# Optimization experiments

Measured on AMD Instinct MI355X. Metric: run time of the kernel, lower is better.

The kernel has to match this reference:

```python
import jax, jax.numpy as jnp
import numpy as np

E = 16      # num_experts
K = 4       # num_experts_per_tok
H = 2048    # hidden_size
I = 1408    # moe_intermediate_size
SI = 5632   # shared expert intermediate size
CAP = 1024
NORM_TOPK = False


def setup_inputs() -> dict:
    key = jax.random.key(0)
    ks = jax.random.split(key, 9)
    def w(k, shape, fan_in):
        return jax.random.normal(k, shape, jnp.float32) * (fan_in ** -0.5)
    return {
        "hidden_states": jax.random.normal(ks[0], (1, 2048, H), jnp.float32),
        "gate_w":  w(ks[1], (E, H), H),        # router: Linear(H -> E), no bias
        "we_gate": w(ks[2], (E, I, H), H),     # per-expert gate_proj weights
        "we_up":   w(ks[3], (E, I, H), H),     # per-expert up_proj weights
        "we_down": w(ks[4], (E, H, I), I),     # per-expert down_proj weights
        "ws_gate": w(ks[5], (SI, H), H),       # shared expert gate_proj
        "ws_up":   w(ks[6], (SI, H), H),       # shared expert up_proj
        "ws_down": w(ks[7], (H, SI), SI),      # shared expert down_proj
        "sg_w":    w(ks[8], (1, H), H),        # shared_expert_gate: Linear(H -> 1)
    }


def reference(hidden_states, gate_w, we_gate, we_up, we_down,
              ws_gate, ws_up, ws_down, sg_w):
    B, S, Hd = hidden_states.shape
    x = hidden_states.reshape(-1, Hd)                      # [T, H]
    T = x.shape[0]

    # --- router ---
    router_logits = x @ gate_w.T                           # [T, E]
    probs = jax.nn.softmax(router_logits.astype(jnp.float32), axis=-1)
    topw, topi = jax.lax.top_k(probs, K)                   # [T, K]
    if NORM_TOPK:
        topw = topw / topw.sum(axis=-1, keepdims=True)

    # --- dispatch: flatten (token, slot) assignments ---
    A = T * K
    fe = topi.reshape(A)                                   # expert id per assignment
    fw = topw.reshape(A)                                   # routing weight per assignment
    ft = jnp.repeat(jnp.arange(T), K)                      # token id per assignment
    # position of each assignment within its expert (rank in arrival order)
    oh = jax.nn.one_hot(fe, E, dtype=jnp.int32)            # [A, E]
    pos = jnp.take_along_axis(jnp.cumsum(oh, axis=0) - 1, fe[:, None], axis=1)[:, 0]
    valid = pos < CAP
    # scatter tokens into per-expert buffers; overflow goes to dummy row CAP
    buf = jnp.zeros((E, CAP + 1, Hd), x.dtype)
    buf = buf.at[fe, jnp.where(valid, pos, CAP)].set(x[ft])[:, :CAP]  # [E, C, H]

    # --- per-expert SiLU-gated MLP (batched grouped GEMMs) ---
    g = jnp.einsum('ech,eih->eci', buf, we_gate)
    u = jnp.einsum('ech,eih->eci', buf, we_up)
    eo = jnp.einsum('eci,ehi->ech', jax.nn.silu(g) * u, we_down)      # [E, C, H]

    # --- combine: weighted scatter-add back to tokens ---
    ga = eo[fe, jnp.minimum(pos, CAP - 1)]                 # [A, H]
    wcomb = (fw * valid.astype(fw.dtype)).astype(x.dtype)
    y = jnp.zeros((T, Hd), x.dtype).at[ft].add(ga * wcomb[:, None])

    # --- shared expert with sigmoid gate ---
    sh = (jax.nn.silu(x @ ws_gate.T) * (x @ ws_up.T)) @ ws_down.T
    sh = jax.nn.sigmoid(x @ sg_w.T) * sh

    out = (y + sh).reshape(B, S, Hd)
    return out, router_logits
```

## Files before the change

kernel.cpp:

```cpp
#include <hip/hip_runtime.h>

#define T_TOK 2048
#define NE 16
#define KTOP 4
#define HD 2048
#define ID 1408
#define SID 5632
#define CAPACITY 1024

typedef __attribute__((ext_vector_type(8))) short short8;
typedef __attribute__((ext_vector_type(4))) float floatx4;

__device__ __forceinline__ short f2b(float f){
  union { float f; unsigned u; } v; v.f = f;
  unsigned r = v.u + 0x7fffu + ((v.u >> 16) & 1u);
  return (short)(r >> 16);
}
__device__ __forceinline__ float b2f(short s){
  union { float f; unsigned u; } v; v.u = ((unsigned)(unsigned short)s) << 16;
  return v.f;
}
__device__ __forceinline__ unsigned cvt_pk(float a, float b){
  unsigned r;
  asm("v_cvt_pk_bf16_f32 %0, %1, %2" : "=v"(r) : "v"(a), "v"(b));
  return r;
}
__device__ __forceinline__ short8 cvt8(float4 a, float4 b){
  union { unsigned d[4]; short8 s; } u;
  u.d[0] = cvt_pk(a.x, a.y); u.d[1] = cvt_pk(a.z, a.w);
  u.d[2] = cvt_pk(b.x, b.y); u.d[3] = cvt_pk(b.z, b.w);
  return u.s;
}
__device__ __forceinline__ void gl16(const void* g, void* l){
  __builtin_amdgcn_global_load_lds(
      (const __attribute__((address_space(1))) void*)g,
      (__attribute__((address_space(3))) void*)l, 16, 0, 0);
}

__device__ __forceinline__ void conv_range(
    int cb, int ncb,
    const float* __restrict__ s1, short* __restrict__ d1, long long n1,
    const float* __restrict__ s2, short* __restrict__ d2, long long n2)
{
  const long long tot = n1 + n2;
  const long long stride = (long long)ncb * 256;
  #pragma unroll 2
  for (long long i = (long long)cb * 256 + threadIdx.x; i < tot; i += stride){
    const float* s; short8* d; long long j;
    if (i < n1){ s = s1; d = (short8*)d1; j = i; }
    else       { s = s2; d = (short8*)d2; j = i - n1; }
    float4 f0 = ((const float4*)s)[j * 2];
    float4 f1 = ((const float4*)s)[j * 2 + 1];
    d[j] = cvt8(f0, f1);
  }
}

__global__ void moe_zero(int* __restrict__ counts){
  if (threadIdx.x < NE) counts[threadIdx.x] = 0;
}

__global__ void moe_router(const float* __restrict__ x,
                           const float* __restrict__ gate_w,
                           const float* __restrict__ sg_w,
                           float* __restrict__ logits_out,
                           short* __restrict__ xb,
                           int* __restrict__ counts,
                           int* __restrict__ slot_token,
                           int* __restrict__ tslot,
                           float* __restrict__ tw,
                           float* __restrict__ sg,
                           const float* cs1, short* cd1, long long cn1,
                           const float* cs2, short* cd2, long long cn2)
{
  if (blockIdx.x >= 512){
    conv_range(blockIdx.x - 512, gridDim.x - 512, cs1, cd1, cn1, cs2, cd2, cn2);
    return;
  }
  int wave = threadIdx.x >> 6, lane = threadIdx.x & 63;
  int t = (blockIdx.x << 2) + wave;
  const float4* xr = (const float4*)(x + (size_t)t * HD);
  short8* xbw = (short8*)(xb + (size_t)t * HD);
  float acc[17];
  #pragma unroll
  for (int e = 0; e < 17; ++e) acc[e] = 0.f;
  #pragma unroll
  for (int j = 0; j < 4; ++j){
    int i4 = (j * 64 + lane) * 2;
    float4 x0 = xr[i4], x1 = xr[i4 + 1];
    xbw[j * 64 + lane] = cvt8(x0, x1);
    #pragma unroll
    for (int e = 0; e < 16; ++e){
      const float4* gr = (const float4*)(gate_w + e * HD);
      float4 g0 = gr[i4], g1 = gr[i4 + 1];
      acc[e] += x0.x*g0.x + x0.y*g0.y + x0.z*g0.z + x0.w*g0.w
              + x1.x*g1.x + x1.y*g1.y + x1.z*g1.z + x1.w*g1.w;
    }
    const float4* sr = (const float4*)sg_w;
    float4 s0 = sr[i4], s1 = sr[i4 + 1];
    acc[16] += x0.x*s0.x + x0.y*s0.y + x0.z*s0.z + x0.w*s0.w
             + x1.x*s1.x + x1.y*s1.y + x1.z*s1.z + x1.w*s1.w;
  }
  #pragma unroll
  for (int e = 0; e < 17; ++e){
    float v = acc[e];
    #pragma unroll
    for (int off = 32; off > 0; off >>= 1) v += __shfl_xor(v, off, 64);
    acc[e] = v;
  }
  if (lane == 0){
    float m = acc[0];
    #pragma unroll
    for (int e = 1; e < 16; ++e) m = fmaxf(m, acc[e]);
    float p[16]; float s = 0.f;
    #pragma unroll
    for (int e = 0; e < 16; ++e){ p[e] = expf(acc[e] - m); s += p[e]; }
    float inv = 1.f / s;
    #pragma unroll
    for (int e = 0; e < 16; ++e) logits_out[t * 16 + e] = acc[e];
    unsigned used = 0;
    for (int k = 0; k < KTOP; ++k){
      float best = -1.f; int bi = 0;
      #pragma unroll
      for (int e = 0; e < 16; ++e){
        float pe = ((used >> e) & 1u) ? -1.f : p[e];
        if (pe > best){ best = pe; bi = e; }
      }
      used |= (1u << bi);
      int pos = atomicAdd(&counts[bi], 1);
      int enc = -1;
      if (pos < CAPACITY){
        slot_token[bi * CAPACITY + pos] = t;
        enc = bi * CAPACITY + pos;
      }
      tslot[t * KTOP + k] = enc;
      tw[t * KTOP + k] = best * inv;
    }
    sg[t] = 1.f / (1.f + expf(-acc[16]));
  }
}


#define GEMM_PREAMBLE \
  const int tid = threadIdx.x; \
  const int lane = tid & 63, wave = tid >> 6; \
  const int wr = wave >> 1, wc = wave & 1; \
  const int lrow = lane & 15, lk = lane >> 4; \
  const int s_th = (tid & 7) ^ ((tid >> 3) & 7); \
  const int koff = (s_th & 3) << 3; \
  const int rloc = ((tid >> 3) << 1) + (s_th >> 2); \
  const int lb = lrow >> 1; \
  const int soff = (((((lrow & 1) << 2) | lk) ^ (lb & 7)) << 4); \
  const int abase = (wr * 32 + lb) * 128 + soff;

#define WAIT8  asm volatile("s_waitcnt vmcnt(8)" ::: "memory");
#define WAIT6  asm volatile("s_waitcnt vmcnt(6)" ::: "memory");
#define WAIT4  asm volatile("s_waitcnt vmcnt(4)" ::: "memory");
#define WAIT3  asm volatile("s_waitcnt vmcnt(3)" ::: "memory");
#define WAIT0  asm volatile("s_waitcnt vmcnt(0)" ::: "memory");
#define SBAR   asm volatile("s_barrier" ::: "memory");

__global__ __launch_bounds__(256) void moe_gateup(
    const short* __restrict__ Asrc,
    const short* __restrict__ Wg, const short* __restrict__ Wu,
    short* __restrict__ Out,
    const int* __restrict__ counts, const int* __restrict__ slot_token,
    int Ndim, int Kdim, int expert_mode, int mtiles, int ntiles,
    const float* cs1, short* cd1, long long cn1,
    const float* cs2, short* cd2, long long cn2, int conv_nwg)
{
  if ((int)blockIdx.x < conv_nwg){
    conv_range(blockIdx.x, conv_nwg, cs1, cd1, cn1, cs2, cd2, cn2);
    return;
  }
  int nwg = gridDim.x - conv_nwg;
  int bid = blockIdx.x - conv_nwg;
  int wg = ((bid & 7) * (nwg >> 3)) + (bid >> 3);
  int m_t = wg % mtiles; wg /= mtiles;
  int n_t = wg % ntiles; int e = wg / ntiles;

  int cnt = T_TOK; size_t woff = 0; short* out = Out;
  if (expert_mode){
    cnt = counts[e]; if (cnt > CAPACITY) cnt = CAPACITY;
    if (m_t * 128 >= cnt) return;
    woff = (size_t)e * Ndim * Kdim;
    out = Out + (size_t)e * CAPACITY * Ndim;
  }
  const int m0 = m_t * 128, n0 = n_t * 64;

  __shared__ __align__(16) char smem[3][16384];

  GEMM_PREAMBLE
  const int gbase = 8192 + (wc * 16 + lb) * 128 + soff;

  const short* aP0;
  const short* aP1;
  {
    int p0 = m0 + rloc, p1 = m0 + 64 + rloc;
    if (expert_mode){
      int q0 = (p0 < cnt) ? p0 : 0, q1 = (p1 < cnt) ? p1 : 0;
      aP0 = Asrc + (size_t)slot_token[e * CAPACITY + q0] * Kdim + koff;
      aP1 = Asrc + (size_t)slot_token[e * CAPACITY + q1] * Kdim + koff;
    } else {
      aP0 = Asrc + (size_t)p0 * Kdim + koff;
      aP1 = Asrc + (size_t)p1 * Kdim + koff;
    }
  }
  const short* bgP = Wg + woff + (size_t)(n0 + rloc) * Kdim + koff;
  const short* buP = Wu + woff + (size_t)(n0 + rloc) * Kdim + koff;

  const floatx4 vzero = {0.f, 0.f, 0.f, 0.f};
  floatx4 accg[4][2], accu[4][2];
  #pragma unroll
  for (int i = 0; i < 4; ++i)
    #pragma unroll
    for (int j = 0; j < 2; ++j){ accg[i][j] = vzero; accu[i][j] = vzero; }

#define GU_ISSUE(B, T) { char* _b = (B); const int _k = (T) << 5; \
    gl16(aP0 + _k, _b + tid * 16); \
    gl16(aP1 + _k, _b + 4096 + tid * 16); \
    gl16(bgP + _k, _b + 8192 + tid * 16); \
    gl16(buP + _k, _b + 12288 + tid * 16); }

#define GU_COMPUTE(B) { const char* bb = (B); \
    short8 a[4], bg[2], bu[2]; \
    _Pragma("unroll") \
    for (int mf = 0; mf < 4; ++mf) a[mf] = *(const short8*)(bb + abase + mf * 1024); \
    _Pragma("unroll") \
    for (int nf = 0; nf < 2; ++nf){ \
      bg[nf] = *(const short8*)(bb + gbase + nf * 1024); \
      bu[nf] = *(const short8*)(bb + gbase + 4096 + nf * 1024); } \
    __builtin_amdgcn_s_setprio(1); \
    _Pragma("unroll") \
    for (int mf = 0; mf < 4; ++mf) \
      _Pragma("unroll") \
      for (int nf = 0; nf < 2; ++nf){ \
        accg[mf][nf] = __builtin_amdgcn_mfma_f32_16x16x32_bf16(a[mf], bg[nf], accg[mf][nf], 0, 0, 0); \
        accu[mf][nf] = __builtin_amdgcn_mfma_f32_16x16x32_bf16(a[mf], bu[nf], accu[mf][nf], 0, 0, 0); } \
    __builtin_amdgcn_s_setprio(0); }

  const int NSTEP = Kdim >> 5;
  char* b0 = smem[0];
  char* b1 = smem[1];
  char* b2 = smem[2];
  GU_ISSUE(b0, 0)
  GU_ISSUE(b1, 1)
  for (int s = 0; s < NSTEP; ++s){
    if (s + 2 < NSTEP){ GU_ISSUE(b2, s + 2) WAIT8 }
    else if (s + 2 == NSTEP){ WAIT4 }
    else { WAIT0 }
    SBAR
    GU_COMPUTE(b0)
    SBAR
    char* t = b0; b0 = b1; b1 = b2; b2 = t;
  }

  const int colbase = n0 + wc * 32 + lrow;
  #pragma unroll
  for (int mf = 0; mf < 4; ++mf){
    int pr = m0 + wr * 64 + mf * 16 + lk * 4;
    #pragma unroll
    for (int nf = 0; nf < 2; ++nf){
      floatx4 g4 = accg[mf][nf], u4 = accu[mf][nf];
      int col = colbase + nf * 16;
      #pragma unroll
      for (int r = 0; r < 4; ++r){
        float gv = g4[r], uv = u4[r];
        float a = (gv / (1.f + __expf(-gv))) * uv;
        out[(size_t)(pr + r) * Ndim + col] = f2b(a);
      }
    }
  }
}

template<int NF>
__global__ __launch_bounds__(256) void moe_down(
    const short* __restrict__ Asrc, const short* __restrict__ Wd,
    float* __restrict__ y, short* __restrict__ eo,
    const int* __restrict__ counts, const int* __restrict__ slot_token,
    const float* __restrict__ sgate,
    int Kdim, int expert_mode, int mtiles, int ntiles)
{
  int nwg = gridDim.x;
  int wg = ((blockIdx.x & 7) * (nwg >> 3)) + (blockIdx.x >> 3);
  int m_t = wg % mtiles; wg /= mtiles;
  int n_t = wg % ntiles; int e = wg / ntiles;

  int cnt = T_TOK; const short* ab = Asrc; size_t woff = 0;
  if (expert_mode){
    cnt = counts[e]; if (cnt > CAPACITY) cnt = CAPACITY;
    if (m_t * 128 >= cnt) return;
    ab = Asrc + (size_t)e * CAPACITY * Kdim;
    woff = (size_t)e * HD * Kdim;
  }
  const int m0 = m_t * 128, n0 = n_t * (NF * 32);

  __shared__ __align__(16) char smem[3][8192 + NF * 2048];

  GEMM_PREAMBLE
  const int bbase = 8192 + (wc * (NF * 8) + lb) * 128 + soff;

  const short* aP0 = ab + (size_t)(m0 + rloc) * Kdim + koff;
  const short* aP1 = ab + (size_t)(m0 + 64 + rloc) * Kdim + koff;
  const short* bP0 = Wd + woff + (size_t)(n0 + rloc) * Kdim + koff;
  const short* bP1 = (NF == 4) ? (Wd + woff + (size_t)(n0 + 64 + rloc) * Kdim + koff) : bP0;

  const floatx4 vzero = {0.f, 0.f, 0.f, 0.f};
  floatx4 acc[4][NF];
  #pragma unroll
  for (int i = 0; i < 4; ++i)
    #pragma unroll
    for (int j = 0; j < NF; ++j) acc[i][j] = vzero;

#define DN_ISSUE(B, T) { char* _b = (B); const int _k = (T) << 5; \
    gl16(aP0 + _k, _b + tid * 16); \
    gl16(aP1 + _k, _b + 4096 + tid * 16); \
    gl16(bP0 + _k, _b + 8192 + tid * 16); \
    if (NF == 4) gl16(bP1 + _k, _b + 12288 + tid * 16); }

#define DN_COMPUTE(B) { const char* bb = (B); \
    short8 a[4], b[NF]; \
    _Pragma("unroll") \
    for (int mf = 0; mf < 4; ++mf) a[mf] = *(const short8*)(bb + abase + mf * 1024); \
    _Pragma("unroll") \
    for (int nf = 0; nf < NF; ++nf) b[nf] = *(const short8*)(bb + bbase + nf * 1024); \
    __builtin_amdgcn_s_setprio(1); \
    _Pragma("unroll") \
    for (int mf = 0; mf < 4; ++mf) \
      _Pragma("unroll") \
      for (int nf = 0; nf < NF; ++nf) \
        acc[mf][nf] = __builtin_amdgcn_mfma_f32_16x16x32_bf16(a[mf], b[nf], acc[mf][nf], 0, 0, 0); \
    __builtin_amdgcn_s_setprio(0); }

  const int NSTEP = Kdim >> 5;
  char* b0 = smem[0];
  char* b1 = smem[1];
  char* b2 = smem[2];
  DN_ISSUE(b0, 0)
  DN_ISSUE(b1, 1)
  for (int s = 0; s < NSTEP; ++s){
    if (s + 2 < NSTEP){
      DN_ISSUE(b2, s + 2)
      if (NF == 4){ WAIT8 } else { WAIT6 }
    } else if (s + 2 == NSTEP){
      if (NF == 4){ WAIT4 } else { WAIT3 }
    } else { WAIT0 }
    SBAR
    DN_COMPUTE(b0)
    SBAR
    char* t = b0; b0 = b1; b1 = b2; b2 = t;
  }

  const int colb = n0 + wc * (NF * 16) + lrow;
  if (expert_mode){
    #pragma unroll
    for (int mf = 0; mf < 4; ++mf){
      int pr = m0 + wr * 64 + mf * 16 + lk * 4;
      #pragma unroll
      for (int r = 0; r < 4; ++r){
        int p = pr + r;
        #pragma unroll
        for (int nf = 0; nf < NF; ++nf)
          eo[(size_t)(e * CAPACITY + p) * HD + colb + nf * 16] = f2b(acc[mf][nf][r]);
      }
    }
  } else {
    #pragma unroll
    for (int mf = 0; mf < 4; ++mf){
      int pr = m0 + wr * 64 + mf * 16 + lk * 4;
      #pragma unroll
      for (int r = 0; r < 4; ++r){
        int t = pr + r;
        float sv = sgate[t];
        #pragma unroll
        for (int nf = 0; nf < NF; ++nf)
          y[(size_t)t * HD + colb + nf * 16] = sv * acc[mf][nf][r];
      }
    }
  }
}

__global__ void moe_combine(const short* __restrict__ eo,
                            const int* __restrict__ tslot,
                            const float* __restrict__ tw,
                            float* __restrict__ y)
{
  int t = blockIdx.x;
  int o = threadIdx.x << 3;
  float* yp = y + (size_t)t * HD + o;
  float4 a0 = *(const float4*)yp, a1 = *(const float4*)(yp + 4);
  float acc[8] = {a0.x, a0.y, a0.z, a0.w, a1.x, a1.y, a1.z, a1.w};
  #pragma unroll
  for (int k = 0; k < KTOP; ++k){
    int s = tslot[t * KTOP + k];
    if (s >= 0){
      float w = tw[t * KTOP + k];
      short8 v = *(const short8*)(eo + (size_t)s * HD + o);
      #pragma unroll
      for (int j = 0; j < 8; ++j) acc[j] += w * b2f(v[j]);
    }
  }
  float4 r0 = {acc[0], acc[1], acc[2], acc[3]};
  float4 r1 = {acc[4], acc[5], acc[6], acc[7]};
  *(float4*)yp = r0; *(float4*)(yp + 4) = r1;
}

extern "C" void kernel_launch(void* const* d_in, const int* in_sizes, int n_in,
                              void* d_out, int out_size, void* d_ws, size_t ws_size,
                              hipStream_t stream)
{
  (void)in_sizes; (void)n_in; (void)out_size; (void)ws_size;
  const float* x       = (const float*)d_in[0];
  const float* gate_w  = (const float*)d_in[1];
  const float* we_gate = (const float*)d_in[2];
  const float* we_up   = (const float*)d_in[3];
  const float* we_down = (const float*)d_in[4];
  const float* wsg     = (const float*)d_in[5];
  const float* wsu     = (const float*)d_in[6];
  const float* wsd     = (const float*)d_in[7];
  const float* sg_w    = (const float*)d_in[8];

  float* y      = (float*)d_out;
  float* logits = y + (size_t)T_TOK * HD;

  const size_t N_EW = (size_t)NE * ID * HD;
  const size_t N_SW = (size_t)SID * HD;
  const long long G_EW = (long long)(N_EW / 8);
  const long long G_SW = (long long)(N_SW / 8);

  char* ws = (char*)d_ws;
  size_t off = 0;
  short* xb   = (short*)(ws + off); off += (size_t)T_TOK * HD * 2;
  short* wb   = (short*)(ws + off); off += (3 * N_EW + 3 * N_SW) * 2;
  short* act  = (short*)(ws + off); off += (size_t)NE * CAPACITY * ID * 2;
  short* acts = (short*)(ws + off); off += (size_t)T_TOK * SID * 2;
  int*   slot_token = (int*)  (ws + off); off += 65536;
  int*   tslot      = (int*)  (ws + off); off += 32768;
  float* tw         = (float*)(ws + off); off += 32768;
  int*   counts     = (int*)  (ws + off); off += 256;
  float* sg         = (float*)(ws + off);

  short* wbeg = wb;
  short* wbeu = wb + N_EW;
  short* wbed = wb + 2 * N_EW;
  short* wbsg = wb + 3 * N_EW;
  short* wbsu = wb + 3 * N_EW + N_SW;
  short* wbsd = wb + 3 * N_EW + 2 * N_SW;
  short* eo = wbeg;

  moe_zero<<<1, 64, 0, stream>>>(counts);
  moe_router<<<512 + 512, 256, 0, stream>>>(x, gate_w, sg_w, logits, xb,
                                            counts, slot_token, tslot, tw, sg,
                                            wsg, wbsg, G_SW, wsu, wbsu, G_SW);
  moe_gateup<<<512 + 16 * 88, 256, 0, stream>>>(xb, wbsg, wbsu, acts,
                                                nullptr, nullptr, SID, HD, 0, 16, 88,
                                                we_gate, wbeg, G_EW, we_up, wbeu, G_EW, 512);
  moe_gateup<<<512 + 8 * 22 * NE, 256, 0, stream>>>(xb, wbeg, wbeu, act,
                                                    counts, slot_token, ID, HD, 1, 8, 22,
                                                    we_down, wbed, G_EW, wsd, wbsd, G_SW, 512);
  moe_down<2><<<16 * 32, 256, 0, stream>>>(acts, wbsd, y, nullptr, nullptr, nullptr,
                                           sg, SID, 0, 16, 32);
  moe_down<4><<<8 * 16 * NE, 256, 0, stream>>>(act, wbed, y, eo, counts, slot_token,
                                               nullptr, ID, 1, 8, 16);
  moe_combine<<<T_TOK, 256, 0, stream>>>(eo, tslot, tw, y);
}
```

Baseline: 760.5 us.

## Merge shared down-projection with expert gate/up into one launch, rebalance conversions

Reorganises the launch schedule. The shared-expert down-projection now runs in the same launch as the routed-expert gate/up GEMM and the expert down-weight conversion, and the shared down-weight fp32-to-bf16 conversion moves into the router launch. The down kernel is specialised to a 128-wide N tile, the count-zeroing kernel becomes a memset, and the number of launches drops. The aim is to cut launch gaps and tail underutilisation by overlapping independent work, at the cost of a mixed-workload grid whose block ordering determines load balance.

```diff
diff --git a/kernel.cpp b/kernel.cpp
--- a/kernel.cpp
+++ b/kernel.cpp
@@ -54,9 +54,24 @@
     d[j] = cvt8(f0, f1);
   }
 }
-
-__global__ void moe_zero(int* __restrict__ counts){
-  if (threadIdx.x < NE) counts[threadIdx.x] = 0;
+__device__ __forceinline__ void conv3(
+    int cb, int ncb,
+    const float* __restrict__ s1, short* __restrict__ d1, long long n1,
+    const float* __restrict__ s2, short* __restrict__ d2, long long n2,
+    const float* __restrict__ s3, short* __restrict__ d3, long long n3)
+{
+  const long long tot = n1 + n2 + n3;
+  const long long stride = (long long)ncb * 256;
+  #pragma unroll 2
+  for (long long i = (long long)cb * 256 + threadIdx.x; i < tot; i += stride){
+    const float* s; short8* d; long long j;
+    if (i < n1){ s = s1; d = (short8*)d1; j = i; }
+    else if (i < n1 + n2){ s = s2; d = (short8*)d2; j = i - n1; }
+    else { s = s3; d = (short8*)d3; j = i - n1 - n2; }
+    float4 f0 = ((const float4*)s)[j * 2];
+    float4 f1 = ((const float4*)s)[j * 2 + 1];
+    d[j] = cvt8(f0, f1);
+  }
 }
 
 __global__ void moe_router(const float* __restrict__ x,
@@ -70,10 +85,11 @@
                            float* __restrict__ tw,
                            float* __restrict__ sg,
                            const float* cs1, short* cd1, long long cn1,
-                           const float* cs2, short* cd2, long long cn2)
+                           const float* cs2, short* cd2, long long cn2,
+                           const float* cs3, short* cd3, long long cn3)
 {
   if (blockIdx.x >= 512){
-    conv_range(blockIdx.x - 512, gridDim.x - 512, cs1, cd1, cn1, cs2, cd2, cn2);
+    conv3(blockIdx.x - 512, gridDim.x - 512, cs1, cd1, cn1, cs2, cd2, cn2, cs3, cd3, cn3);
     return;
   }
   int wave = threadIdx.x >> 6, lane = threadIdx.x & 63;
@@ -153,27 +169,19 @@
   const int abase = (wr * 32 + lb) * 128 + soff;
 
 #define WAIT8  asm volatile("s_waitcnt vmcnt(8)" ::: "memory");
-#define WAIT6  asm volatile("s_waitcnt vmcnt(6)" ::: "memory");
 #define WAIT4  asm volatile("s_waitcnt vmcnt(4)" ::: "memory");
-#define WAIT3  asm volatile("s_waitcnt vmcnt(3)" ::: "memory");
 #define WAIT0  asm volatile("s_waitcnt vmcnt(0)" ::: "memory");
 #define SBAR   asm volatile("s_barrier" ::: "memory");
 
-__global__ __launch_bounds__(256) void moe_gateup(
+__device__ __forceinline__ void dev_gateup(
+    char (&smem)[3][16384],
     const short* __restrict__ Asrc,
     const short* __restrict__ Wg, const short* __restrict__ Wu,
     short* __restrict__ Out,
     const int* __restrict__ counts, const int* __restrict__ slot_token,
     int Ndim, int Kdim, int expert_mode, int mtiles, int ntiles,
-    const float* cs1, short* cd1, long long cn1,
-    const float* cs2, short* cd2, long long cn2, int conv_nwg)
-{
-  if ((int)blockIdx.x < conv_nwg){
-    conv_range(blockIdx.x, conv_nwg, cs1, cd1, cn1, cs2, cd2, cn2);
-    return;
-  }
-  int nwg = gridDim.x - conv_nwg;
-  int bid = blockIdx.x - conv_nwg;
+    int bid, int nwg)
+{
   int wg = ((bid & 7) * (nwg >> 3)) + (bid >> 3);
   int m_t = wg % mtiles; wg /= mtiles;
   int n_t = wg % ntiles; int e = wg / ntiles;
@@ -186,8 +194,6 @@
     out = Out + (size_t)e * CAPACITY * Ndim;
   }
   const int m0 = m_t * 128, n0 = n_t * 64;
-
-  __shared__ __align__(16) char smem[3][16384];
 
   GEMM_PREAMBLE
   const int gbase = 8192 + (wc * 16 + lb) * 128 + soff;
@@ -272,16 +278,15 @@
   }
 }
 
-template<int NF>
-__global__ __launch_bounds__(256) void moe_down(
+__device__ __forceinline__ void dev_down4(
+    char (&smem)[3][16384],
     const short* __restrict__ Asrc, const short* __restrict__ Wd,
     float* __restrict__ y, short* __restrict__ eo,
     const int* __restrict__ counts, const int* __restrict__ slot_token,
     const float* __restrict__ sgate,
-    int Kdim, int expert_mode, int mtiles, int ntiles)
-{
-  int nwg = gridDim.x;
-  int wg = ((blockIdx.x & 7) * (nwg >> 3)) + (blockIdx.x >> 3);
+    int Kdim, int expert_mode, int mtiles, int ntiles, int bid, int nwg)
+{
+  int wg = ((bid & 7) * (nwg >> 3)) + (bid >> 3);
   int m_t = wg % mtiles; wg /= mtiles;
   int n_t = wg % ntiles; int e = wg / ntiles;
 
@@ -292,42 +297,40 @@
     ab = Asrc + (size_t)e * CAPACITY * Kdim;
     woff = (size_t)e * HD * Kdim;
   }
-  const int m0 = m_t * 128, n0 = n_t * (NF * 32);
-
-  __shared__ __align__(16) char smem[3][8192 + NF * 2048];
+  const int m0 = m_t * 128, n0 = n_t * 128;
 
   GEMM_PREAMBLE
-  const int bbase = 8192 + (wc * (NF * 8) + lb) * 128 + soff;
+  const int bbase = 8192 + (wc * 32 + lb) * 128 + soff;
 
   const short* aP0 = ab + (size_t)(m0 + rloc) * Kdim + koff;
   const short* aP1 = ab + (size_t)(m0 + 64 + rloc) * Kdim + koff;
   const short* bP0 = Wd + woff + (size_t)(n0 + rloc) * Kdim + koff;
-  const short* bP1 = (NF == 4) ? (Wd + woff + (size_t)(n0 + 64 + rloc) * Kdim + koff) : bP0;
+  const short* bP1 = Wd + woff + (size_t)(n0 + 64 + rloc) * Kdim + koff;
 
   const floatx4 vzero = {0.f, 0.f, 0.f, 0.f};
-  floatx4 acc[4][NF];
+  floatx4 acc[4][4];
   #pragma unroll
   for (int i = 0; i < 4; ++i)
     #pragma unroll
-    for (int j = 0; j < NF; ++j) acc[i][j] = vzero;
+    for (int j = 0; j < 4; ++j) acc[i][j] = vzero;
 
 #define DN_ISSUE(B, T) { char* _b = (B); const int _k = (T) << 5; \
     gl16(aP0 + _k, _b + tid * 16); \
     gl16(aP1 + _k, _b + 4096 + tid * 16); \
     gl16(bP0 + _k, _b + 8192 + tid * 16); \
-    if (NF == 4) gl16(bP1 + _k, _b + 12288 + tid * 16); }
+    gl16(bP1 + _k, _b + 12288 + tid * 16); }
 
 #define DN_COMPUTE(B) { const char* bb = (B); \
-    short8 a[4], b[NF]; \
+    short8 a[4], b[4]; \
     _Pragma("unroll") \
     for (int mf = 0; mf < 4; ++mf) a[mf] = *(const short8*)(bb + abase + mf * 1024); \
     _Pragma("unroll") \
-    for (int nf = 0; nf < NF; ++nf) b[nf] = *(const short8*)(bb + bbase + nf * 1024); \
+    for (int nf = 0; nf < 4; ++nf) b[nf] = *(const short8*)(bb + bbase + nf * 1024); \
     __builtin_amdgcn_s_setprio(1); \
     _Pragma("unroll") \
     for (int mf = 0; mf < 4; ++mf) \
       _Pragma("unroll") \
-      for (int nf = 0; nf < NF; ++nf) \
+      for (int nf = 0; nf < 4; ++nf) \
         acc[mf][nf] = __builtin_amdgcn_mfma_f32_16x16x32_bf16(a[mf], b[nf], acc[mf][nf], 0, 0, 0); \
     __builtin_amdgcn_s_setprio(0); }
 
@@ -338,19 +341,16 @@
   DN_ISSUE(b0, 0)
   DN_ISSUE(b1, 1)
   for (int s = 0; s < NSTEP; ++s){
-    if (s + 2 < NSTEP){
-      DN_ISSUE(b2, s + 2)
-      if (NF == 4){ WAIT8 } else { WAIT6 }
-    } else if (s + 2 == NSTEP){
-      if (NF == 4){ WAIT4 } else { WAIT3 }
-    } else { WAIT0 }
+    if (s + 2 < NSTEP){ DN_ISSUE(b2, s + 2) WAIT8 }
+    else if (s + 2 == NSTEP){ WAIT4 }
+    else { WAIT0 }
     SBAR
     DN_COMPUTE(b0)
     SBAR
     char* t = b0; b0 = b1; b1 = b2; b2 = t;
   }
 
-  const int colb = n0 + wc * (NF * 16) + lrow;
+  const int colb = n0 + wc * 64 + lrow;
   if (expert_mode){
     #pragma unroll
     for (int mf = 0; mf < 4; ++mf){
@@ -359,7 +359,7 @@
       for (int r = 0; r < 4; ++r){
         int p = pr + r;
         #pragma unroll
-        for (int nf = 0; nf < NF; ++nf)
+        for (int nf = 0; nf < 4; ++nf)
           eo[(size_t)(e * CAPACITY + p) * HD + colb + nf * 16] = f2b(acc[mf][nf][r]);
       }
     }
@@ -372,11 +372,63 @@
         int t = pr + r;
         float sv = sgate[t];
         #pragma unroll
-        for (int nf = 0; nf < NF; ++nf)
+        for (int nf = 0; nf < 4; ++nf)
           y[(size_t)t * HD + colb + nf * 16] = sv * acc[mf][nf][r];
       }
     }
   }
+}
+
+__global__ __launch_bounds__(256) void moe_gateup_sh(
+    const short* __restrict__ xb,
+    const short* __restrict__ wbsg, const short* __restrict__ wbsu,
+    short* __restrict__ acts,
+    const float* cs1, short* cd1, long long cn1,
+    const float* cs2, short* cd2, long long cn2, int conv_nwg)
+{
+  __shared__ __align__(16) char smem[3][16384];
+  if ((int)blockIdx.x < conv_nwg){
+    conv_range(blockIdx.x, conv_nwg, cs1, cd1, cn1, cs2, cd2, cn2);
+    return;
+  }
+  dev_gateup(smem, xb, wbsg, wbsu, acts, nullptr, nullptr, SID, HD, 0, 16, 88,
+             blockIdx.x - conv_nwg, gridDim.x - conv_nwg);
+}
+
+__global__ __launch_bounds__(256) void moe_mid(
+    const short* __restrict__ xb,
+    const short* __restrict__ wbeg, const short* __restrict__ wbeu,
+    short* __restrict__ act,
+    const short* __restrict__ acts, const short* __restrict__ wbsd,
+    float* __restrict__ y, const float* __restrict__ sg,
+    const int* __restrict__ counts, const int* __restrict__ slot_token,
+    const float* ed, short* wbed, long long n_ed)
+{
+  __shared__ __align__(16) char smem[3][16384];
+  int bx = blockIdx.x;
+  if (bx < 512){
+    conv_range(bx, 512, ed, wbed, n_ed, nullptr, nullptr, 0);
+    return;
+  }
+  bx -= 512;
+  if (bx < 256){
+    dev_down4(smem, acts, wbsd, y, nullptr, nullptr, nullptr, sg,
+              SID, 0, 16, 16, bx, 256);
+    return;
+  }
+  bx -= 256;
+  dev_gateup(smem, xb, wbeg, wbeu, act, counts, slot_token, ID, HD, 1, 8, 22,
+             bx, 2816);
+}
+
+__global__ __launch_bounds__(256) void moe_down_ex(
+    const short* __restrict__ act, const short* __restrict__ wbed,
+    float* __restrict__ y, short* __restrict__ eo,
+    const int* __restrict__ counts, const int* __restrict__ slot_token)
+{
+  __shared__ __align__(16) char smem[3][16384];
+  dev_down4(smem, act, wbed, y, eo, counts, slot_token, nullptr,
+            ID, 1, 8, 16, blockIdx.x, gridDim.x);
 }
 
 __global__ void moe_combine(const short* __restrict__ eo,
@@ -447,19 +499,18 @@
   short* wbsd = wb + 3 * N_EW + 2 * N_SW;
   short* eo = wbeg;
 
-  moe_zero<<<1, 64, 0, stream>>>(counts);
-  moe_router<<<512 + 512, 256, 0, stream>>>(x, gate_w, sg_w, logits, xb,
-                                            counts, slot_token, tslot, tw, sg,
-                                            wsg, wbsg, G_SW, wsu, wbsu, G_SW);
-  moe_gateup<<<512 + 16 * 88, 256, 0, stream>>>(xb, wbsg, wbsu, acts,
-                                                nullptr, nullptr, SID, HD, 0, 16, 88,
-                                                we_gate, wbeg, G_EW, we_up, wbeu, G_EW, 512);
-  moe_gateup<<<512 + 8 * 22 * NE, 256, 0, stream>>>(xb, wbeg, wbeu, act,
-                                                    counts, slot_token, ID, HD, 1, 8, 22,
-                                                    we_down, wbed, G_EW, wsd, wbsd, G_SW, 512);
-  moe_down<2><<<16 * 32, 256, 0, stream>>>(acts, wbsd, y, nullptr, nullptr, nullptr,
-                                           sg, SID, 0, 16, 32);
-  moe_down<4><<<8 * 16 * NE, 256, 0, stream>>>(act, wbed, y, eo, counts, slot_token,
-                                               nullptr, ID, 1, 8, 16);
+  hipMemsetAsync(counts, 0, 64, stream);
+  moe_router<<<512 + 1024, 256, 0, stream>>>(x, gate_w, sg_w, logits, xb,
+                                             counts, slot_token, tslot, tw, sg,
+                                             wsg, wbsg, G_SW, wsu, wbsu, G_SW,
+                                             wsd, wbsd, G_SW);
+  moe_gateup_sh<<<512 + 16 * 88, 256, 0, stream>>>(xb, wbsg, wbsu, acts,
+                                                   we_gate, wbeg, G_EW,
+                                                   we_up, wbeu, G_EW, 512);
+  moe_mid<<<512 + 256 + 2816, 256, 0, stream>>>(xb, wbeg, wbeu, act,
+                                                acts, wbsd, y, sg,
+                                                counts, slot_token,
+                                                we_down, wbed, G_EW);
+  moe_down_ex<<<8 * 16 * NE, 256, 0, stream>>>(act, wbed, y, eo, counts, slot_token);
   moe_combine<<<T_TOK, 256, 0, stream>>>(eo, tslot, tw, y);
 }
```

Result: faster. 735.3 us, median of 2 (-3.3%).
